# Kernel optimization log

Hardware: AMD Instinct MI355X
Metric: run time of the kernel (lower is better)

## Reference

```python
import jax, jax.numpy as jnp
import numpy as np

B, N, E, D, L, NC = 48, 96, 1024, 300, 4, 7
NEG = 1e30


def _gru(x, h, w_ih, w_hh, b_ih, b_hh):
    # torch.nn.GRUCell math; weights are (3D, D) in torch layout
    gi = x @ w_ih.T + b_ih
    gh = h @ w_hh.T + b_hh
    ir, iz, inn = jnp.split(gi, 3, axis=-1)
    hr, hz, hn = jnp.split(gh, 3, axis=-1)
    r = jax.nn.sigmoid(ir + hr)
    z = jax.nn.sigmoid(iz + hz)
    n = jnp.tanh(inn + r * hn)
    return (1.0 - z) * n + z * h


def _layer(Cin, Hin, adj, cwi, cwh, cbi, cbh, pwi, pwh, pbi, pbh, wq, wk, gb):
    b, n, d = Cin.shape
    zeros = jnp.zeros((b, d), Cin.dtype)
    c0 = _gru(Cin[:, 0], zeros, cwi, cwh, cbi, cbh)          # GRUCell with h=0
    p0 = _gru(zeros, Cin[:, 0], pwi, pwh, pbi, pbh)          # M=0 at step 0
    P0 = jnp.zeros_like(Cin).at[:, 0].set(p0)                # growing P kept as full buffer
    pos = jnp.arange(n)

    def step(P, i):
        q = Cin[:, i]                                        # (B, D)
        mask = adj[:, i] * (pos < i).astype(adj.dtype)       # only predecessors j < i
        # GatLinear: Linear(cat(Q,K)) == Q.wq + K.wk + b
        alpha = (q @ wq)[:, None] + P @ wk + gb              # (B, N)
        alpha = alpha - (1.0 - mask) * NEG                   # mask_logic
        w = jax.nn.softmax(alpha, axis=-1)
        M = jnp.einsum('bn,bnd->bd', w, P)
        c_i = _gru(q, M, cwi, cwh, cbi, cbh)
        p_i = _gru(M, Hin[:, i], pwi, pwh, pbi, pbh)
        P = jax.lax.dynamic_update_slice(P, p_i[:, None, :], (0, i, 0))
        return P, c_i

    P, Cs = jax.lax.scan(step, P0, jnp.arange(1, n))
    CL = jnp.concatenate([c0[:, None], jnp.moveaxis(Cs, 0, 1)], axis=1)  # (B, N, D)
    return CL, P


def reference(features, adj, s_mask, fc1_w, fc1_b,
              gc_wih, gc_whh, gc_bih, gc_bhh,
              gp_wih, gp_whh, gp_bih, gp_bhh,
              gat_wq, gat_wk, gat_b,
              mlp_w0, mlp_b0, mlp_w1, mlp_b1, mlp_w2, mlp_b2):
    # s_mask is unused when no_rel_attn=True (faithful to torch forward)
    H0 = jax.nn.relu(features @ fc1_w + fc1_b)
    H_list = [H0]
    C_list = [H0]
    for l in range(L):
        CL, P = _layer(C_list[l], H_list[l], adj,
                       gc_wih[l], gc_whh[l], gc_bih[l], gc_bhh[l],
                       gp_wih[l], gp_whh[l], gp_bih[l], gp_bhh[l],
                       gat_wq[l], gat_wk[l], gat_b[l])
        C_list.append(CL)
        H_list.append(CL)
        H_list.append(P)
    H_list.append(features)
    H = jnp.concatenate(H_list, axis=2)                      # (B, N, 9D + E)
    x = jax.nn.relu(H @ mlp_w0 + mlp_b0)
    x = jax.nn.relu(x @ mlp_w1 + mlp_b1)
    logits = x @ mlp_w2 + mlp_b2                             # (B, N, NC)
    return logits


def setup_inputs() -> dict:
    key = jax.random.key(0)
    ks = jax.random.split(key, 25)
    s = 0.02

    def p(k, shape):
        return jax.random.normal(k, shape, jnp.float32) * s

    features = jax.random.normal(ks[0], (B, N, E), jnp.float32)
    # DAG adjacency: random predecessors, strictly lower-triangular, previous
    # utterance always connected (guarantees a nonempty attention context)
    base = jax.random.bernoulli(ks[1], 0.5, (B, N, N)).astype(jnp.float32)
    tri = jnp.tril(jnp.ones((N, N), jnp.float32), -1)
    prev = jnp.eye(N, k=-1, dtype=jnp.float32)
    adj = jnp.maximum(base * tri, prev[None])
    s_mask = jax.random.randint(ks[2], (B, N, N), 0, 2, jnp.int32)
    in_dim = D * (2 * L + 1) + E
    return {
        'features': features, 'adj': adj, 's_mask': s_mask,
        'fc1_w': p(ks[3], (E, D)), 'fc1_b': p(ks[4], (D,)),
        'gc_wih': p(ks[5], (L, 3 * D, D)), 'gc_whh': p(ks[6], (L, 3 * D, D)),
        'gc_bih': p(ks[7], (L, 3 * D)), 'gc_bhh': p(ks[8], (L, 3 * D)),
        'gp_wih': p(ks[9], (L, 3 * D, D)), 'gp_whh': p(ks[10], (L, 3 * D, D)),
        'gp_bih': p(ks[11], (L, 3 * D)), 'gp_bhh': p(ks[12], (L, 3 * D)),
        'gat_wq': p(ks[13], (L, D)), 'gat_wk': p(ks[14], (L, D)), 'gat_b': p(ks[15], (L,)),
        'mlp_w0': p(ks[16], (in_dim, D)), 'mlp_b0': p(ks[17], (D,)),
        'mlp_w1': p(ks[18], (D, D)), 'mlp_b1': p(ks[19], (D,)),
        'mlp_w2': p(ks[20], (D, NC)), 'mlp_b2': p(ks[21], (NC,)),
    }
```

## Files before the change

### kernel.cpp

```cpp
#include <hip/hip_runtime.h>
#include <math.h>

#define BB 48
#define NN 96
#define EE 1024
#define DD 300
#define LL 4
#define G3 900
#define PP 150
#define PP2 152
#define NC4 38
#define HDIM 3724
#define ROWS (BB*NN)
#define NEGI -1.0e30f
#define KP300 304
#define GIC_TILES 540

typedef _Float16 half2_t __attribute__((ext_vector_type(2)));
typedef _Float16 h8 __attribute__((ext_vector_type(8)));
typedef float f4 __attribute__((ext_vector_type(4)));

__device__ __forceinline__ float sigm(float x){ return 1.0f/(1.0f+expf(-x)); }

__device__ __forceinline__ void dot4(const h8 wv, const h8 mc,
                                     float& a0, float& a1, float& a2, float& a3)
{
    half2_t w0,w1,w2,w3,m0,m1,m2,m3;
    w0.x=wv[0]; w0.y=wv[1]; m0.x=mc[0]; m0.y=mc[1];
    w1.x=wv[2]; w1.y=wv[3]; m1.x=mc[2]; m1.y=mc[3];
    w2.x=wv[4]; w2.y=wv[5]; m2.x=mc[4]; m2.y=mc[5];
    w3.x=wv[6]; w3.y=wv[7]; m3.x=mc[6]; m3.y=mc[7];
    a0 = __builtin_amdgcn_fdot2(w0, m0, a0, false);
    a1 = __builtin_amdgcn_fdot2(w1, m1, a1, false);
    a2 = __builtin_amdgcn_fdot2(w2, m2, a2, false);
    a3 = __builtin_amdgcn_fdot2(w3, m3, a3, false);
}

__global__ __launch_bounds__(256) void pack_w_q(const float* __restrict__ src_all,
                                                h8* __restrict__ dst)
{
    int l = blockIdx.y;
    int idx = blockIdx.x*256 + threadIdx.x;
    if (idx >= NC4*G3) return;
    int c = idx / G3, gate = idx % G3;
    const float* src = src_all + (size_t)l*G3*DD + (size_t)gate*DD;
    h8 v;
    #pragma unroll
    for (int j=0;j<8;j++){
        int d = 8*c + j;
        v[j] = (d<DD) ? (_Float16)src[d] : (_Float16)0.f;
    }
    dst[(size_t)l*NC4*G3 + idx] = v;
}

__global__ __launch_bounds__(256) void conv_gru_w(const float* __restrict__ gp_whh,
                                                  const float* __restrict__ gc_wih,
                                                  const float* __restrict__ gc_whh,
                                                  _Float16* __restrict__ outp)
{
    int z = blockIdx.y; int l = z/3, wsel = z%3;
    const float* src = (wsel==0?gp_whh:wsel==1?gc_wih:gc_whh) + (size_t)l*G3*DD;
    _Float16* dst = outp + (size_t)z*G3*KP300;
    int idx = blockIdx.x*256 + threadIdx.x;
    if (idx >= G3*KP300) return;
    int n = idx/KP300, k = idx%KP300;
    dst[idx] = (k<DD) ? (_Float16)src[(size_t)n*DD+k] : (_Float16)0.f;
}

__global__ __launch_bounds__(256) void convT(const float* __restrict__ src,
                                             _Float16* __restrict__ dst,
                                             int K, int N, int Kpad)
{
    int idx = blockIdx.x*256 + threadIdx.x;
    if (idx >= N*Kpad) return;
    int n = idx/Kpad, k = idx%Kpad;
    dst[idx] = (k<K) ? (_Float16)src[(size_t)k*N + n] : (_Float16)0.f;
}

__device__ __forceinline__ void gemm_tile(
    int m0, int n0, int tid,
    const float* __restrict__ A, int lda,
    const _Float16* __restrict__ B, int Kpad,
    const float* __restrict__ bias,
    float* __restrict__ C, int ldc,
    int N, int K, int relu)
{
    constexpr int KPS=40;
    __shared__ _Float16 As[128][KPS];
    __shared__ _Float16 Bs[64][KPS];
    int w = tid>>6, lane = tid&63;
    int wy = w>>1, wx = w&1;
    int lm = lane&15, q = lane>>4;

    f4 acc[4][2];
    #pragma unroll
    for (int a=0;a<4;a++)
        #pragma unroll
        for (int b=0;b<2;b++)
            #pragma unroll
            for (int r=0;r<4;r++) acc[a][b][r]=0.f;

    int am = tid>>1, akg = (tid&1)*16;
    int bn = tid>>2, bkg = (tid&3)*8;
    const float* arow = A + (size_t)(m0+am)*lda;

    for (int k0=0; k0<K; k0+=32){
        {
            __align__(16) _Float16 av[16];
            #pragma unroll
            for (int u=0;u<16;u+=4){
                int k = k0 + akg + u;
                float x0,x1,x2,x3;
                if (k+4 <= K){
                    float4 v = *(const float4*)(arow + k);
                    x0=v.x;x1=v.y;x2=v.z;x3=v.w;
                } else {
                    x0 = (k  <K)? arow[k  ]:0.f;
                    x1 = (k+1<K)? arow[k+1]:0.f;
                    x2 = (k+2<K)? arow[k+2]:0.f;
                    x3 = (k+3<K)? arow[k+3]:0.f;
                }
                av[u]=(_Float16)x0; av[u+1]=(_Float16)x1;
                av[u+2]=(_Float16)x2; av[u+3]=(_Float16)x3;
            }
            *(h8*)&As[am][akg]   = *(h8*)&av[0];
            *(h8*)&As[am][akg+8] = *(h8*)&av[8];
        }
        {
            int gk = k0 + bkg;
            h8 bv;
            #pragma unroll
            for (int j=0;j<8;j++) bv[j]=(_Float16)0.f;
            if (n0+bn < N && gk < Kpad)
                bv = *(const h8*)(B + (size_t)(n0+bn)*Kpad + gk);
            *(h8*)&Bs[bn][bkg] = bv;
        }
        __syncthreads();
        h8 af[4], bf[2];
        #pragma unroll
        for (int mb=0; mb<4; mb++) af[mb] = *(h8*)&As[wy*64+mb*16+lm][q*8];
        #pragma unroll
        for (int nb=0; nb<2; nb++) bf[nb] = *(h8*)&Bs[wx*32+nb*16+lm][q*8];
        #pragma unroll
        for (int mb=0; mb<4; mb++)
            #pragma unroll
            for (int nb=0; nb<2; nb++)
                acc[mb][nb] = __builtin_amdgcn_mfma_f32_16x16x32_f16(af[mb], bf[nb], acc[mb][nb], 0,0,0);
        __syncthreads();
    }
    #pragma unroll
    for (int mb=0; mb<4; mb++){
        int r0 = m0 + wy*64 + mb*16 + q*4;
        #pragma unroll
        for (int nb=0; nb<2; nb++){
            int c = n0 + wx*32 + nb*16 + lm;
            if (c < N){
                float bb = bias[c];
                #pragma unroll
                for (int reg=0; reg<4; reg++){
                    float v = acc[mb][nb][reg] + bb;
                    if (relu) v = fmaxf(v, 0.f);
                    C[(size_t)(r0+reg)*ldc + c] = v;
                }
            }
        }
    }
}

__global__ __launch_bounds__(256) void gemm_mfma(
    const float* __restrict__ A, int lda,
    const _Float16* __restrict__ B, int Kpad,
    const float* __restrict__ bias,
    float* __restrict__ C, int ldc,
    int N, int K, int relu)
{
    gemm_tile(blockIdx.y*128, blockIdx.x*64, threadIdx.x,
              A, lda, B, Kpad, bias, C, ldc, N, K, relu);
}

__global__ void featcopy(const float* __restrict__ f, float* __restrict__ H)
{
    size_t row = blockIdx.x;
    int t = threadIdx.x;
    float4 v = *(const float4*)(f + row*EE + t*4);
    *(float4*)(H + row*HDIM + 2700 + t*4) = v;
}

__global__ __launch_bounds__(1024, 4) void scan_kernel(
    float* __restrict__ Hbuf,
    const float* __restrict__ GHp,
    const h8* __restrict__ pwiQ,
    const h8* __restrict__ pwhQ,
    const float* __restrict__ pbi,
    const float* __restrict__ pbh,
    const float* __restrict__ wk,
    const float* __restrict__ wq,
    const float* __restrict__ gat_b, int lidx,
    const float* __restrict__ adj,
    float* __restrict__ Mbuf,
    int ccol, int hcol, int pcol,
    const _Float16* __restrict__ cwiF,
    const float* __restrict__ cbi,
    float* __restrict__ GIc)
{
    if (blockIdx.x >= BB){
        if (threadIdx.x < 256){
            int bid = blockIdx.x - BB;
            int n0 = (bid % 15)*64, m0 = (bid / 15)*128;
            gemm_tile(m0, n0, threadIdx.x, Hbuf + ccol, HDIM, cwiF, KP300,
                      cbi, GIc, G3, G3, DD, 0);
        }
        return;
    }

    int b = blockIdx.x;
    int t = threadIdx.x;

    __shared__ __align__(16) half2_t P_h2[NN][PP];
    __shared__ __align__(16) float g_s[G3];
    __shared__ __align__(16) float Mpart[3][DD];
    __shared__ __align__(16) half2_t M_h2[PP2];
    __shared__ __align__(16) float e_s[NN];
    __shared__ __align__(16) float pk_s[NN];
    __shared__ __align__(16) float pw_s[DD];
    __shared__ __align__(16) float adj_s[NN*NN];
    __shared__ __align__(16) float qd_s[NN];
    __shared__ __align__(16) float ghp_s[G3];
    __shared__ __align__(16) float hv_s[DD];

    size_t rowbase = (size_t)b*NN;

    h8 wr0,wr1,wr2,wr3,wr4,wr5,wr6,wr7,wr8,wr9,wr10,wr11;
    float pbi_r = 0.f;
    if (t < G3){
        const h8* W = pwiQ + t;
        wr0 = W[0];        wr1 = W[(size_t)1*G3];  wr2 = W[(size_t)2*G3];
        wr3 = W[(size_t)3*G3];  wr4 = W[(size_t)4*G3];  wr5 = W[(size_t)5*G3];
        wr6 = W[(size_t)6*G3];  wr7 = W[(size_t)7*G3];  wr8 = W[(size_t)8*G3];
        wr9 = W[(size_t)9*G3];  wr10 = W[(size_t)10*G3]; wr11 = W[(size_t)11*G3];
        pbi_r = pbi[t];
    }
    float2 wk_r = make_float2(0.f,0.f);
    if (t < PP) wk_r = *(const float2*)&wk[2*t];

    for (int k=t; k<NN*NN; k+=1024) adj_s[k] = adj[rowbase*NN + k];
    {
        int w = t>>6, lane = t&63;
        float gb = gat_b[lidx];
        for (int r = w; r < NN; r += 16){
            const float* x = Hbuf + (rowbase + r)*HDIM + ccol;
            float s = 0.f;
            for (int d=lane; d<DD; d+=64) s += x[d]*wq[d];
            #pragma unroll
            for (int o=32;o>0;o>>=1) s += __shfl_xor(s,o);
            if (lane==0) qd_s[r] = s + gb;
        }
    }
    if (t < PP){
        float2 c2 = *(const float2*)&Hbuf[rowbase*HDIM + ccol + 2*t];
        Mpart[0][2*t] = c2.x; Mpart[0][2*t+1] = c2.y;
        half2_t mh; mh.x = (_Float16)c2.x; mh.y = (_Float16)c2.y;
        M_h2[t] = mh;
    } else if (t < PP2){
        half2_t z; z.x=(_Float16)0.f; z.y=(_Float16)0.f;
        M_h2[t] = z;
    }
    __syncthreads();
    if (t < G3){
        const h8* W = pwhQ + t;
        float a0=0.f, a1=0.f, a2=0.f, a3=0.f;
        #pragma unroll 4
        for (int c=0;c<NC4;c++){
            h8 wv = W[(size_t)c*G3];
            h8 mc = *(h8*)&M_h2[4*c];
            dot4(wv, mc, a0,a1,a2,a3);
        }
        g_s[t] = pbh[t] + (a0+a2) + (a1+a3);
    }
    __syncthreads();
    if (t < PP){
        int d0 = 2*t, d1 = 2*t+1;
        float r0  = sigm(pbi[d0]      + g_s[d0]);
        float z0  = sigm(pbi[DD+d0]   + g_s[DD+d0]);
        float n0  = tanhf(pbi[2*DD+d0] + r0*g_s[2*DD+d0]);
        float p0  = (1.f-z0)*n0 + z0*Mpart[0][d0];
        float r1  = sigm(pbi[d1]      + g_s[d1]);
        float z1  = sigm(pbi[DD+d1]   + g_s[DD+d1]);
        float n1  = tanhf(pbi[2*DD+d1] + r1*g_s[2*DD+d1]);
        float p1  = (1.f-z1)*n1 + z1*Mpart[0][d1];
        *(float2*)&Hbuf[rowbase*HDIM + pcol + d0] = make_float2(p0,p1);
        half2_t ph; ph.x = (_Float16)p0; ph.y = (_Float16)p1;
        P_h2[0][t] = ph;
        pw_s[d0] = p0*wk_r.x;
        pw_s[d1] = p1*wk_r.y;
        *(float2*)&Mbuf[rowbase*DD + d0] = make_float2(0.f,0.f);
    }
    __syncthreads();

    for (int i=1;i<NN;i++){
        size_t row = rowbase + i;
        if (t < 64){
            float s = 0.f;
            for (int c=t;c<DD;c+=64) s += pw_s[c];
            #pragma unroll
            for (int o=32;o>0;o>>=1) s += __shfl_xor(s,o);
            if (t==0) pk_s[i-1] = s;
            float q = qd_s[i];
            float a0 = NEGI, a1 = NEGI;
            if (t < i){
                if (adj_s[i*NN+t] != 0.f) a0 = q + ((t==i-1)? s : pk_s[t]);
            }
            int j1 = 64+t;
            if (t < 32 && j1 < i){
                if (adj_s[i*NN+j1] != 0.f) a1 = q + ((j1==i-1)? s : pk_s[j1]);
            }
            float m = fmaxf(a0,a1);
            #pragma unroll
            for (int o=32;o>0;o>>=1) m = fmaxf(m, __shfl_xor(m,o));
            float e0 = expf(a0-m);
            float e1 = (t<32)? expf(a1-m) : 0.f;
            float ss = e0+e1;
            #pragma unroll
            for (int o=32;o>0;o>>=1) ss += __shfl_xor(ss,o);
            float inv = 1.f/ss;
            e_s[t] = e0*inv;
            if (t<32) e_s[64+t] = e1*inv;
        }
        __syncthreads();
        if (t < 450){
            int g = t/150, dp = t%150;
            int cnt = (i+2)/3;
            int j0 = g*cnt; int j1 = j0+cnt; if (j1 > i) j1 = i;
            float m0=0.f, m1=0.f;
            for (int j=j0;j<j1;j++){
                float w = e_s[j];
                half2_t pv = P_h2[j][dp];
                m0 += w*(float)pv.x;
                m1 += w*(float)pv.y;
            }
            *(float2*)&Mpart[g][2*dp] = make_float2(m0,m1);
        } else if (t >= 512){
            int k = t-512;
            #pragma unroll
            for (int it=0; it<2; it++){
                int idx = k + it*512;
                if (idx < 450){
                    *(float2*)&ghp_s[2*idx] = *(const float2*)&GHp[row*G3 + 2*idx];
                } else if (idx < 600){
                    int h = idx-450;
                    *(float2*)&hv_s[2*h] = *(const float2*)&Hbuf[row*HDIM + hcol + 2*h];
                }
            }
        }
        __syncthreads();
        if (t < PP){
            float m0 = Mpart[0][2*t] + Mpart[1][2*t] + Mpart[2][2*t];
            float m1 = Mpart[0][2*t+1] + Mpart[1][2*t+1] + Mpart[2][2*t+1];
            half2_t mh; mh.x = (_Float16)m0; mh.y = (_Float16)m1;
            M_h2[t] = mh;
            *(float2*)&Mbuf[row*DD + 2*t] = make_float2(m0,m1);
        }
        __syncthreads();
        if (t < G3){
            const h8* W = pwiQ + t;
            float a0=0.f, a1=0.f, a2=0.f, a3=0.f;
            dot4(wr0,  *(h8*)&M_h2[0],  a0,a1,a2,a3);
            dot4(wr1,  *(h8*)&M_h2[4],  a0,a1,a2,a3);
            dot4(wr2,  *(h8*)&M_h2[8],  a0,a1,a2,a3);
            dot4(wr3,  *(h8*)&M_h2[12], a0,a1,a2,a3);
            dot4(wr4,  *(h8*)&M_h2[16], a0,a1,a2,a3);
            dot4(wr5,  *(h8*)&M_h2[20], a0,a1,a2,a3);
            dot4(wr6,  *(h8*)&M_h2[24], a0,a1,a2,a3);
            dot4(wr7,  *(h8*)&M_h2[28], a0,a1,a2,a3);
            dot4(wr8,  *(h8*)&M_h2[32], a0,a1,a2,a3);
            dot4(wr9,  *(h8*)&M_h2[36], a0,a1,a2,a3);
            dot4(wr10, *(h8*)&M_h2[40], a0,a1,a2,a3);
            dot4(wr11, *(h8*)&M_h2[44], a0,a1,a2,a3);
            #pragma unroll 4
            for (int c=12;c<NC4;c++){
                h8 wv = W[(size_t)c*G3];
                h8 mc = *(h8*)&M_h2[4*c];
                dot4(wv, mc, a0,a1,a2,a3);
            }
            g_s[t] = pbi_r + (a0+a2) + (a1+a3);
        }
        __syncthreads();
        if (t < PP){
            int d0 = 2*t, d1 = 2*t+1;
            float2 hv = *(const float2*)&hv_s[d0];
            float r0  = sigm(g_s[d0]      + ghp_s[d0]);
            float z0  = sigm(g_s[DD+d0]   + ghp_s[DD+d0]);
            float n0  = tanhf(g_s[2*DD+d0] + r0*ghp_s[2*DD+d0]);
            float p0  = (1.f-z0)*n0 + z0*hv.x;
            float r1  = sigm(g_s[d1]      + ghp_s[d1]);
            float z1  = sigm(g_s[DD+d1]   + ghp_s[DD+d1]);
            float n1  = tanhf(g_s[2*DD+d1] + r1*ghp_s[2*DD+d1]);
            float p1  = (1.f-z1)*n1 + z1*hv.y;
            *(float2*)&Hbuf[row*HDIM + pcol + d0] = make_float2(p0,p1);
            half2_t ph; ph.x = (_Float16)p0; ph.y = (_Float16)p1;
            P_h2[i][t] = ph;
            pw_s[d0] = p0*wk_r.x;
            pw_s[d1] = p1*wk_r.y;
        }
        __syncthreads();
    }
}

__global__ __launch_bounds__(320) void combine_c(
    const float* __restrict__ GIc, const float* __restrict__ GHc,
    const float* __restrict__ Mbuf, float* __restrict__ Hbuf, int clcol)
{
    size_t row = blockIdx.x;
    int d = threadIdx.x;
    if (d < DD){
        float ir = GIc[row*G3+d], iz = GIc[row*G3+DD+d], inn = GIc[row*G3+2*DD+d];
        float hr = GHc[row*G3+d], hz = GHc[row*G3+DD+d], hn  = GHc[row*G3+2*DD+d];
        float r  = sigm(ir+hr);
        float z  = sigm(iz+hz);
        float nn = tanhf(inn + r*hn);
        float h  = Mbuf[row*DD+d];
        Hbuf[row*HDIM + clcol + d] = (1.f-z)*nn + z*h;
    }
}

__global__ __launch_bounds__(64) void logits_kernel(
    const float* __restrict__ x2, const float* __restrict__ w2,
    const float* __restrict__ b2, float* __restrict__ out)
{
    size_t row = blockIdx.x;
    int lane = threadIdx.x;
    float acc[7]={0,0,0,0,0,0,0};
    for (int d=lane; d<DD; d+=64){
        float x = x2[row*DD+d];
        #pragma unroll
        for (int c=0;c<7;c++) acc[c] += x*w2[d*7+c];
    }
    #pragma unroll
    for (int c=0;c<7;c++){
        float s = acc[c];
        #pragma unroll
        for (int o=32;o>0;o>>=1) s += __shfl_down(s,o);
        if (lane==0) out[row*7+c] = s + b2[c];
    }
}

extern "C" void kernel_launch(void* const* d_in, const int* in_sizes, int n_in,
                              void* d_out, int out_size, void* d_ws, size_t ws_size,
                              hipStream_t stream)
{
    const float* features = (const float*)d_in[0];
    const float* adj      = (const float*)d_in[1];
    const float* fc1_w    = (const float*)d_in[3];
    const float* fc1_b    = (const float*)d_in[4];
    const float* gc_wih   = (const float*)d_in[5];
    const float* gc_whh   = (const float*)d_in[6];
    const float* gc_bih   = (const float*)d_in[7];
    const float* gc_bhh   = (const float*)d_in[8];
    const float* gp_wih   = (const float*)d_in[9];
    const float* gp_whh   = (const float*)d_in[10];
    const float* gp_bih   = (const float*)d_in[11];
    const float* gp_bhh   = (const float*)d_in[12];
    const float* gat_wq   = (const float*)d_in[13];
    const float* gat_wk   = (const float*)d_in[14];
    const float* gat_b    = (const float*)d_in[15];
    const float* mlp_w0   = (const float*)d_in[16];
    const float* mlp_b0   = (const float*)d_in[17];
    const float* mlp_w1   = (const float*)d_in[18];
    const float* mlp_b1   = (const float*)d_in[19];
    const float* mlp_w2   = (const float*)d_in[20];
    const float* mlp_b2   = (const float*)d_in[21];
    float* out = (float*)d_out;

    float* ws = (float*)d_ws;
    size_t off = 0;
    float* Hbuf = ws + off; off += (size_t)ROWS*HDIM;
    float* bufA = ws + off; off += (size_t)ROWS*G3;
    float* bufB = ws + off; off += (size_t)ROWS*G3;
    float* bufC = ws + off; off += (size_t)ROWS*G3;
    float* Mbuf = ws + off; off += (size_t)ROWS*DD;
    h8* pwiQ = (h8*)(ws + off); off += (size_t)LL*NC4*G3*4;
    h8* pwhQ = (h8*)(ws + off); off += (size_t)LL*NC4*G3*4;
    _Float16* gruF = (_Float16*)(ws + off); off += (size_t)12*G3*KP300/2;
    _Float16* fc1F = (_Float16*)(ws + off); off += (size_t)DD*EE/2;
    _Float16* mlp0F= (_Float16*)(ws + off); off += (size_t)DD*3728/2;
    _Float16* mlp1F= (_Float16*)(ws + off); off += (size_t)DD*KP300/2;
    (void)ws_size; (void)in_sizes; (void)n_in; (void)out_size;

    {
        pack_w_q<<<dim3((NC4*G3+255)/256, LL), 256, 0, stream>>>(gp_wih, pwiQ);
        pack_w_q<<<dim3((NC4*G3+255)/256, LL), 256, 0, stream>>>(gp_whh, pwhQ);
        conv_gru_w<<<dim3((G3*KP300+255)/256, 12), 256, 0, stream>>>(gp_whh, gc_wih, gc_whh, gruF);
        convT<<<(DD*EE+255)/256, 256, 0, stream>>>(fc1_w, fc1F, EE, DD, EE);
        convT<<<(DD*3728+255)/256, 256, 0, stream>>>(mlp_w0, mlp0F, HDIM, DD, 3728);
        convT<<<(DD*KP300+255)/256, 256, 0, stream>>>(mlp_w1, mlp1F, DD, DD, KP300);
    }
    gemm_mfma<<<dim3(5,36),256,0,stream>>>(features, EE, fc1F, EE, fc1_b,
                                           Hbuf, HDIM, DD, EE, 1);
    featcopy<<<ROWS,256,0,stream>>>(features, Hbuf);

    for (int l=0;l<LL;l++){
        int ccol  = (l==0)? 0 : 300 + (l-1)*600;
        int hcol  = l*300;
        int pcol  = 600 + l*600;
        int clcol = 300 + l*600;
        const h8* pwiQl = pwiQ + (size_t)l*NC4*G3;
        const h8* pwhQl = pwhQ + (size_t)l*NC4*G3;
        const _Float16* pwhF = gruF + (size_t)(l*3+0)*G3*KP300;
        const _Float16* cwiF = gruF + (size_t)(l*3+1)*G3*KP300;
        const _Float16* cwhF = gruF + (size_t)(l*3+2)*G3*KP300;

        gemm_mfma<<<dim3(15,36),256,0,stream>>>(Hbuf+hcol, HDIM, pwhF, KP300,
                                                gp_bhh + l*G3, bufA, G3, G3, DD, 0);
        scan_kernel<<<BB+GIC_TILES,1024,0,stream>>>(Hbuf, bufA, pwiQl, pwhQl,
                                          gp_bih + l*G3, gp_bhh + l*G3,
                                          gat_wk + l*DD, gat_wq + l*DD, gat_b, l,
                                          adj, Mbuf, ccol, hcol, pcol,
                                          cwiF, gc_bih + l*G3, bufB);
        gemm_mfma<<<dim3(15,36),256,0,stream>>>(Mbuf, DD, cwhF, KP300,
                                                gc_bhh + l*G3, bufC, G3, G3, DD, 0);
        combine_c<<<ROWS,320,0,stream>>>(bufB, bufC, Mbuf, Hbuf, clcol);
    }

    gemm_mfma<<<dim3(5,36),256,0,stream>>>(Hbuf, HDIM, mlp0F, 3728, mlp_b0,
                                           bufB, DD, DD, HDIM, 1);
    gemm_mfma<<<dim3(5,36),256,0,stream>>>(bufB, DD, mlp1F, KP300, mlp_b1,
                                           bufC, DD, DD, DD, 1);
    logits_kernel<<<ROWS,64,0,stream>>>(bufC, mlp_w2, mlp_b2, out);
}
```

Before: 3.194 ms.

## Fuse context GRU hidden GEMM with gate combine; simplify scan M reduction

Replaces the separate hidden-state GEMM and combine_c kernel with one MFMA kernel that computes all three gate tiles per output column and applies the GRU update in its epilogue, so the GHc buffer is never written and read back. Inside the scan loop, the attention-weighted sum over P is now done by 150 threads over all predecessors instead of a 3-way split plus a reduction, which removes one barrier per step but lengthens the serial loop per thread. The two weight-packing launches are merged into one. The scan change trades parallelism for fewer syncs and could slow the latency-bound recurrence.

```diff
diff --git a/kernel.cpp b/kernel.cpp
--- a/kernel.cpp
+++ b/kernel.cpp
@@ -36,10 +36,14 @@
     a3 = __builtin_amdgcn_fdot2(w3, m3, a3, false);
 }
 
-__global__ __launch_bounds__(256) void pack_w_q(const float* __restrict__ src_all,
-                                                h8* __restrict__ dst)
-{
-    int l = blockIdx.y;
+__global__ __launch_bounds__(256) void pack_w_q8(const float* __restrict__ gp_wih,
+                                                 const float* __restrict__ gp_whh,
+                                                 h8* __restrict__ pwiQ,
+                                                 h8* __restrict__ pwhQ)
+{
+    int z = blockIdx.y; int l = z>>1, which = z&1;
+    const float* src_all = which ? gp_whh : gp_wih;
+    h8* dst = which ? pwhQ : pwiQ;
     int idx = blockIdx.x*256 + threadIdx.x;
     if (idx >= NC4*G3) return;
     int c = idx / G3, gate = idx % G3;
@@ -176,6 +180,109 @@
 {
     gemm_tile(blockIdx.y*128, blockIdx.x*64, threadIdx.x,
               A, lda, B, Kpad, bias, C, ldc, N, K, relu);
+}
+
+__global__ __launch_bounds__(256) void ghc_fused(
+    const float* __restrict__ Mbuf,
+    const _Float16* __restrict__ cwhF,
+    const float* __restrict__ cbh,
+    const float* __restrict__ GIc,
+    float* __restrict__ Hbuf, int clcol)
+{
+    constexpr int KPS=40;
+    __shared__ _Float16 As[128][KPS];
+    __shared__ _Float16 Bs[3][64][KPS];
+    int tid = threadIdx.x;
+    int m0 = blockIdx.y*128, n0 = blockIdx.x*64;
+    int w = tid>>6, lane = tid&63;
+    int wy = w>>1, wx = w&1;
+    int lm = lane&15, q = lane>>4;
+
+    f4 acc[3][4][2];
+    #pragma unroll
+    for (int g=0;g<3;g++)
+        #pragma unroll
+        for (int a=0;a<4;a++)
+            #pragma unroll
+            for (int b=0;b<2;b++)
+                #pragma unroll
+                for (int r=0;r<4;r++) acc[g][a][b][r]=0.f;
+
+    int am = tid>>1, akg = (tid&1)*16;
+    int bn = tid>>2, bkg = (tid&3)*8;
+    const float* arow = Mbuf + (size_t)(m0+am)*DD;
+
+    for (int k0=0; k0<DD; k0+=32){
+        {
+            __align__(16) _Float16 av[16];
+            #pragma unroll
+            for (int u=0;u<16;u+=4){
+                int k = k0 + akg + u;
+                float x0,x1,x2,x3;
+                if (k+4 <= DD){
+                    float4 v = *(const float4*)(arow + k);
+                    x0=v.x;x1=v.y;x2=v.z;x3=v.w;
+                } else {
+                    x0 = (k  <DD)? arow[k  ]:0.f;
+                    x1 = (k+1<DD)? arow[k+1]:0.f;
+                    x2 = (k+2<DD)? arow[k+2]:0.f;
+                    x3 = (k+3<DD)? arow[k+3]:0.f;
+                }
+                av[u]=(_Float16)x0; av[u+1]=(_Float16)x1;
+                av[u+2]=(_Float16)x2; av[u+3]=(_Float16)x3;
+            }
+            *(h8*)&As[am][akg]   = *(h8*)&av[0];
+            *(h8*)&As[am][akg+8] = *(h8*)&av[8];
+        }
+        {
+            int gk = k0 + bkg;
+            #pragma unroll
+            for (int g=0; g<3; g++){
+                h8 bv;
+                #pragma unroll
+                for (int j=0;j<8;j++) bv[j]=(_Float16)0.f;
+                if (n0+bn < DD && gk < KP300)
+                    bv = *(const h8*)(cwhF + (size_t)(g*300 + n0+bn)*KP300 + gk);
+                *(h8*)&Bs[g][bn][bkg] = bv;
+            }
+        }
+        __syncthreads();
+        h8 af[4];
+        #pragma unroll
+        for (int mb=0; mb<4; mb++) af[mb] = *(h8*)&As[wy*64+mb*16+lm][q*8];
+        #pragma unroll
+        for (int g=0; g<3; g++){
+            h8 bf0 = *(h8*)&Bs[g][wx*32+lm][q*8];
+            h8 bf1 = *(h8*)&Bs[g][wx*32+16+lm][q*8];
+            #pragma unroll
+            for (int mb=0; mb<4; mb++){
+                acc[g][mb][0] = __builtin_amdgcn_mfma_f32_16x16x32_f16(af[mb], bf0, acc[g][mb][0], 0,0,0);
+                acc[g][mb][1] = __builtin_amdgcn_mfma_f32_16x16x32_f16(af[mb], bf1, acc[g][mb][1], 0,0,0);
+            }
+        }
+        __syncthreads();
+    }
+    #pragma unroll
+    for (int mb=0; mb<4; mb++){
+        int r0 = m0 + wy*64 + mb*16 + q*4;
+        #pragma unroll
+        for (int nb=0; nb<2; nb++){
+            int c = n0 + wx*32 + nb*16 + lm;
+            if (c < DD){
+                float br = cbh[c], bz = cbh[300+c], bn2 = cbh[600+c];
+                #pragma unroll
+                for (int reg=0; reg<4; reg++){
+                    int rowi = r0 + reg;
+                    const float* gi = GIc + (size_t)rowi*G3;
+                    float r = sigm(gi[c]     + acc[0][mb][nb][reg] + br);
+                    float z = sigm(gi[300+c] + acc[1][mb][nb][reg] + bz);
+                    float n = tanhf(gi[600+c] + r*(acc[2][mb][nb][reg] + bn2));
+                    float hprev = Mbuf[(size_t)rowi*DD + c];
+                    Hbuf[(size_t)rowi*HDIM + clcol + c] = (1.f-z)*n + z*hprev;
+                }
+            }
+        }
+    }
 }
 
 __global__ void featcopy(const float* __restrict__ f, float* __restrict__ H)
@@ -218,7 +325,6 @@
 
     __shared__ __align__(16) half2_t P_h2[NN][PP];
     __shared__ __align__(16) float g_s[G3];
-    __shared__ __align__(16) float Mpart[3][DD];
     __shared__ __align__(16) half2_t M_h2[PP2];
     __shared__ __align__(16) float e_s[NN];
     __shared__ __align__(16) float pk_s[NN];
@@ -258,7 +364,6 @@
     }
     if (t < PP){
         float2 c2 = *(const float2*)&Hbuf[rowbase*HDIM + ccol + 2*t];
-        Mpart[0][2*t] = c2.x; Mpart[0][2*t+1] = c2.y;
         half2_t mh; mh.x = (_Float16)c2.x; mh.y = (_Float16)c2.y;
         M_h2[t] = mh;
     } else if (t < PP2){
@@ -280,14 +385,15 @@
     __syncthreads();
     if (t < PP){
         int d0 = 2*t, d1 = 2*t+1;
+        float2 c2 = *(const float2*)&Hbuf[rowbase*HDIM + ccol + d0];
         float r0  = sigm(pbi[d0]      + g_s[d0]);
         float z0  = sigm(pbi[DD+d0]   + g_s[DD+d0]);
         float n0  = tanhf(pbi[2*DD+d0] + r0*g_s[2*DD+d0]);
-        float p0  = (1.f-z0)*n0 + z0*Mpart[0][d0];
+        float p0  = (1.f-z0)*n0 + z0*c2.x;
         float r1  = sigm(pbi[d1]      + g_s[d1]);
         float z1  = sigm(pbi[DD+d1]   + g_s[DD+d1]);
         float n1  = tanhf(pbi[2*DD+d1] + r1*g_s[2*DD+d1]);
-        float p1  = (1.f-z1)*n1 + z1*Mpart[0][d1];
+        float p1  = (1.f-z1)*n1 + z1*c2.y;
         *(float2*)&Hbuf[rowbase*HDIM + pcol + d0] = make_float2(p0,p1);
         half2_t ph; ph.x = (_Float16)p0; ph.y = (_Float16)p1;
         P_h2[0][t] = ph;
@@ -327,38 +433,30 @@
             if (t<32) e_s[64+t] = e1*inv;
         }
         __syncthreads();
-        if (t < 450){
-            int g = t/150, dp = t%150;
-            int cnt = (i+2)/3;
-            int j0 = g*cnt; int j1 = j0+cnt; if (j1 > i) j1 = i;
+        if (t < PP){
             float m0=0.f, m1=0.f;
-            for (int j=j0;j<j1;j++){
+            #pragma unroll 4
+            for (int j=0;j<i;j++){
                 float w = e_s[j];
-                half2_t pv = P_h2[j][dp];
+                half2_t pv = P_h2[j][t];
                 m0 += w*(float)pv.x;
                 m1 += w*(float)pv.y;
             }
-            *(float2*)&Mpart[g][2*dp] = make_float2(m0,m1);
-        } else if (t >= 512){
-            int k = t-512;
-            #pragma unroll
-            for (int it=0; it<2; it++){
-                int idx = k + it*512;
-                if (idx < 450){
-                    *(float2*)&ghp_s[2*idx] = *(const float2*)&GHp[row*G3 + 2*idx];
-                } else if (idx < 600){
-                    int h = idx-450;
-                    *(float2*)&hv_s[2*h] = *(const float2*)&Hbuf[row*HDIM + hcol + 2*h];
-                }
-            }
-        }
-        __syncthreads();
-        if (t < PP){
-            float m0 = Mpart[0][2*t] + Mpart[1][2*t] + Mpart[2][2*t];
-            float m1 = Mpart[0][2*t+1] + Mpart[1][2*t+1] + Mpart[2][2*t+1];
             half2_t mh; mh.x = (_Float16)m0; mh.y = (_Float16)m1;
             M_h2[t] = mh;
             *(float2*)&Mbuf[row*DD + 2*t] = make_float2(m0,m1);
+        } else if (t >= 512){
+            int idx = t-512;
+            #pragma unroll
+            for (int it=0; it<2; it++){
+                int id2 = idx + it*512;
+                if (id2 < 450){
+                    *(float2*)&ghp_s[2*id2] = *(const float2*)&GHp[row*G3 + 2*id2];
+                } else if (id2 < 600){
+                    int hh = id2-450;
+                    *(float2*)&hv_s[2*hh] = *(const float2*)&Hbuf[row*HDIM + hcol + 2*hh];
+                }
+            }
         }
         __syncthreads();
         if (t < G3){
@@ -403,23 +501,6 @@
             pw_s[d1] = p1*wk_r.y;
         }
         __syncthreads();
-    }
-}
-
-__global__ __launch_bounds__(320) void combine_c(
-    const float* __restrict__ GIc, const float* __restrict__ GHc,
-    const float* __restrict__ Mbuf, float* __restrict__ Hbuf, int clcol)
-{
-    size_t row = blockIdx.x;
-    int d = threadIdx.x;
-    if (d < DD){
-        float ir = GIc[row*G3+d], iz = GIc[row*G3+DD+d], inn = GIc[row*G3+2*DD+d];
-        float hr = GHc[row*G3+d], hz = GHc[row*G3+DD+d], hn  = GHc[row*G3+2*DD+d];
-        float r  = sigm(ir+hr);
-        float z  = sigm(iz+hz);
-        float nn = tanhf(inn + r*hn);
-        float h  = Mbuf[row*DD+d];
-        Hbuf[row*HDIM + clcol + d] = (1.f-z)*nn + z*h;
     }
 }
 
@@ -487,8 +568,7 @@
     (void)ws_size; (void)in_sizes; (void)n_in; (void)out_size;
 
     {
-        pack_w_q<<<dim3((NC4*G3+255)/256, LL), 256, 0, stream>>>(gp_wih, pwiQ);
-        pack_w_q<<<dim3((NC4*G3+255)/256, LL), 256, 0, stream>>>(gp_whh, pwhQ);
+        pack_w_q8<<<dim3((NC4*G3+255)/256, 2*LL), 256, 0, stream>>>(gp_wih, gp_whh, pwiQ, pwhQ);
         conv_gru_w<<<dim3((G3*KP300+255)/256, 12), 256, 0, stream>>>(gp_whh, gc_wih, gc_whh, gruF);
         convT<<<(DD*EE+255)/256, 256, 0, stream>>>(fc1_w, fc1F, EE, DD, EE);
         convT<<<(DD*3728+255)/256, 256, 0, stream>>>(mlp_w0, mlp0F, HDIM, DD, 3728);
@@ -516,9 +596,8 @@
                                           gat_wk + l*DD, gat_wq + l*DD, gat_b, l,
                                           adj, Mbuf, ccol, hcol, pcol,
                                           cwiF, gc_bih + l*G3, bufB);
-        gemm_mfma<<<dim3(15,36),256,0,stream>>>(Mbuf, DD, cwhF, KP300,
-                                                gc_bhh + l*G3, bufC, G3, G3, DD, 0);
-        combine_c<<<ROWS,320,0,stream>>>(bufB, bufC, Mbuf, Hbuf, clcol);
+        ghc_fused<<<dim3(5,36),256,0,stream>>>(Mbuf, cwhF, gc_bhh + l*G3,
+                                               bufB, Hbuf, clcol);
     }
 
     gemm_mfma<<<dim3(5,36),256,0,stream>>>(Hbuf, HDIM, mlp0F, 3728, mlp_b0,
```

Result: slower. 3.274 ms (+2.5%).
